# Performance work log

Measured on AMD Instinct MI355X. Metric: run time of the kernel, lower is better.

Reference implementation:

```python
import jax, jax.numpy as jnp
import numpy as np

B, S, H = 1, 1024, 2048
NH, NKV, HD = 32, 4, 128
E, K, I = 32, 8, 768
EPS = 1e-6
THETA = 10000.0


def setup_inputs() -> dict:
    key = jax.random.key(0)
    ks = jax.random.split(key, 12)
    s = 0.02
    return {
        "x": jax.random.normal(ks[0], (B, S, H), jnp.float32),
        "ln1_w": jnp.ones((H,), jnp.float32),
        "ln2_w": jnp.ones((H,), jnp.float32),
        "q_norm_w": jnp.ones((HD,), jnp.float32),
        "k_norm_w": jnp.ones((HD,), jnp.float32),
        "Wq": jax.random.normal(ks[1], (H, NH * HD), jnp.float32) * s,
        "Wk": jax.random.normal(ks[2], (H, NKV * HD), jnp.float32) * s,
        "Wv": jax.random.normal(ks[3], (H, NKV * HD), jnp.float32) * s,
        "Wo": jax.random.normal(ks[4], (NH * HD, H), jnp.float32) * s,
        "Wg": jax.random.normal(ks[5], (H, E), jnp.float32) * s,
        "W_gate_up": jax.random.normal(ks[6], (E, H, 2 * I), jnp.float32) * s,
        "W_down": jax.random.normal(ks[7], (E, I, H), jnp.float32) * s,
    }


def rms_norm(x, w, eps=EPS):
    var = jnp.mean(jnp.square(x), axis=-1, keepdims=True)
    return x * jax.lax.rsqrt(var + eps) * w


def rotate_half(x):
    x1, x2 = jnp.split(x, 2, axis=-1)
    return jnp.concatenate([-x2, x1], axis=-1)


def rope_cos_sin(seq_len, dtype):
    inv_freq = 1.0 / (THETA ** (jnp.arange(0, HD, 2, dtype=jnp.float32) / HD))
    freqs = jnp.arange(seq_len, dtype=jnp.float32)[:, None] * inv_freq[None, :]
    emb = jnp.concatenate([freqs, freqs], axis=-1)  # [S, HD]
    return jnp.cos(emb).astype(dtype)[None, :, None, :], jnp.sin(emb).astype(dtype)[None, :, None, :]


def attention(h, q_norm_w, k_norm_w, Wq, Wk, Wv, Wo):
    b, s, _ = h.shape
    q = (h @ Wq).reshape(b, s, NH, HD)
    k = (h @ Wk).reshape(b, s, NKV, HD)
    v = (h @ Wv).reshape(b, s, NKV, HD)
    # Qwen3 per-head q/k RMSNorm
    q = rms_norm(q, q_norm_w)
    k = rms_norm(k, k_norm_w)
    cos, sin = rope_cos_sin(s, h.dtype)
    q = q * cos + rotate_half(q) * sin
    k = k * cos + rotate_half(k) * sin
    # GQA: repeat kv heads
    rep = NH // NKV
    k = jnp.repeat(k, rep, axis=2)
    v = jnp.repeat(v, rep, axis=2)
    scale = HD ** -0.5
    scores = jnp.einsum('bqhd,bkhd->bhqk', q, k) * scale
    mask = jnp.tril(jnp.ones((s, s), bool))
    scores = jnp.where(mask[None, None], scores, jnp.array(-1e9, scores.dtype))
    attn = jax.nn.softmax(scores, axis=-1)
    out = jnp.einsum('bhqk,bkhd->bqhd', attn, v).reshape(b, s, NH * HD)
    return out @ Wo


def moe(h, Wg, W_gate_up, W_down):
    b, s, _ = h.shape
    t = h.reshape(b * s, H)
    logits = t @ Wg                          # [T, E]
    probs = jax.nn.softmax(logits, axis=-1)
    weights, indices = jax.lax.top_k(probs, K)  # [T, K] (no renormalization, per TopKRouter)
    combine = jnp.sum(jax.nn.one_hot(indices, E, dtype=t.dtype) * weights[..., None], axis=1)  # [T, E]
    gu = jnp.einsum('th,ehf->etf', t, W_gate_up)     # [E, T, 2I]
    gate, up = jnp.split(gu, 2, axis=-1)
    act = jax.nn.silu(gate) * up                     # [E, T, I]
    y = jnp.einsum('eti,eih->eth', act, W_down)      # [E, T, H]
    out = jnp.einsum('eth,te->th', y, combine)
    return out.reshape(b, s, H)


def reference(x, ln1_w, ln2_w, q_norm_w, k_norm_w, Wq, Wk, Wv, Wo, Wg, W_gate_up, W_down):
    h = x + attention(rms_norm(x, ln1_w), q_norm_w, k_norm_w, Wq, Wk, Wv, Wo)
    out = h + moe(rms_norm(h, ln2_w), Wg, W_gate_up, W_down)
    return out
```

## Files before the change

kernel.cpp:

```cpp
#include <hip/hip_runtime.h>
#include <hip/hip_bf16.h>


#define T_TOK 1024
#define HDIM  2048
#define NHEAD 32
#define NKVH  4
#define HD    128
#define NEXP  32
#define TOPK  8
#define IDIM  768

typedef __hip_bfloat16 bf16;

__device__ __forceinline__ float ld1(const float* p, size_t i) { return p[i]; }
__device__ __forceinline__ float ld1(const bf16* p, size_t i) { return __bfloat162float(p[i]); }

__global__ void detect_kernel(const unsigned* __restrict__ ln1w_bits, int* __restrict__ flag) {
  if (threadIdx.x == 0) flag[0] = (ln1w_bits[0] == 0x3F803F80u) ? 1 : 0;
}

template <typename Tx, typename Tw>
__device__ __forceinline__ void rms_body(const Tx* __restrict__ x, const Tw* __restrict__ w,
                                         float* __restrict__ out, float* red) {
  int t = blockIdx.x;
  const Tx* row = x + (size_t)t * HDIM;
  float ss = 0.f;
  for (int h = threadIdx.x; h < HDIM; h += 256) {
    float v = ld1(row, h);
    ss += v * v;
  }
#pragma unroll
  for (int off = 32; off; off >>= 1) ss += __shfl_down(ss, off);
  if ((threadIdx.x & 63) == 0) red[threadIdx.x >> 6] = ss;
  __syncthreads();
  float inv = rsqrtf((red[0] + red[1] + red[2] + red[3]) / (float)HDIM + 1e-6f);
  float* o = out + (size_t)t * HDIM;
  for (int h = threadIdx.x; h < HDIM; h += 256) o[h] = ld1(row, h) * inv * ld1(w, h);
}

__global__ void rmsnorm_dyn_kernel(const void* x, const void* w, float* out, const int* flag) {
  __shared__ float red[4];
  if (flag[0]) rms_body<bf16, bf16>((const bf16*)x, (const bf16*)w, out, red);
  else         rms_body<float, float>((const float*)x, (const float*)w, out, red);
}

__global__ void rmsnorm_f32_kernel(const float* x, const void* w, float* out, const int* flag) {
  __shared__ float red[4];
  if (flag[0]) rms_body<float, bf16>(x, (const bf16*)w, out, red);
  else         rms_body<float, float>(x, (const float*)w, out, red);
}

template <typename Tb>
__device__ __forceinline__ void gemm_body(const float* __restrict__ A, const Tb* __restrict__ B,
                                          float* __restrict__ C, const Tb* __restrict__ res,
                                          int N, int K, float* As , float* Bs) {
  int tid = threadIdx.x;
  int tx = tid & 15, ty = tid >> 4;
  int row0 = blockIdx.y * 64, col0 = blockIdx.x * 64;
  float acc[4][4] = {};
  for (int k0 = 0; k0 < K; k0 += 16) {
#pragma unroll
    for (int l = 0; l < 4; ++l) {
      int idx = tid + l * 256;
      int r = idx >> 4, c = idx & 15;
      As[c * 65 + r] = A[(size_t)(row0 + r) * K + k0 + c];
    }
#pragma unroll
    for (int l = 0; l < 4; ++l) {
      int idx = tid + l * 256;
      int r = idx >> 6, c = idx & 63;
      Bs[r * 65 + c] = ld1(B, (size_t)(k0 + r) * N + col0 + c);
    }
    __syncthreads();
#pragma unroll
    for (int k = 0; k < 16; ++k) {
      float av[4], bv[4];
#pragma unroll
      for (int i = 0; i < 4; ++i) av[i] = As[k * 65 + ty * 4 + i];
#pragma unroll
      for (int j = 0; j < 4; ++j) bv[j] = Bs[k * 65 + tx * 4 + j];
#pragma unroll
      for (int i = 0; i < 4; ++i)
#pragma unroll
        for (int j = 0; j < 4; ++j) acc[i][j] += av[i] * bv[j];
    }
    __syncthreads();
  }
#pragma unroll
  for (int i = 0; i < 4; ++i) {
    int r = row0 + ty * 4 + i;
#pragma unroll
    for (int j = 0; j < 4; ++j) {
      int c = col0 + tx * 4 + j;
      float v = acc[i][j];
      if (res) v += ld1(res, (size_t)r * N + c);
      C[(size_t)r * N + c] = v;
    }
  }
}

__global__ void gemm_kernel(const float* A, const void* B, float* C, const void* res,
                            int N, int K, const int* flag) {
  __shared__ float As[16 * 65];
  __shared__ float Bs[16 * 65];
  if (flag[0]) gemm_body<bf16>(A, (const bf16*)B, C, (const bf16*)res, N, K, As, Bs);
  else         gemm_body<float>(A, (const float*)B, C, (const float*)res, N, K, As, Bs);
}

template <typename Tw>
__device__ __forceinline__ void qkrope_body(float* __restrict__ q, float* __restrict__ k,
                                            const Tw* __restrict__ qw, const Tw* __restrict__ kw,
                                            float* sred, float* sh) {
  int t = blockIdx.x;
  int head = blockIdx.y;
  float* vec;
  const Tw* w;
  if (head < NHEAD) {
    vec = q + ((size_t)t * NHEAD + head) * HD;
    w = qw;
  } else {
    vec = k + ((size_t)t * NKVH + (head - NHEAD)) * HD;
    w = kw;
  }
  int d = threadIdx.x;
  float v = vec[d];
  float ss = v * v;
#pragma unroll
  for (int off = 32; off; off >>= 1) ss += __shfl_down(ss, off);
  if ((d & 63) == 0) sred[d >> 6] = ss;
  __syncthreads();
  float inv = rsqrtf((sred[0] + sred[1]) / (float)HD + 1e-6f);
  float nv = v * inv * ld1(w, d);
  sh[d] = nv;
  __syncthreads();
  float other = (d < 64) ? -sh[d + 64] : sh[d - 64];
  float inv_freq = powf(10000.f, -(float)(d & 63) / 64.f);
  float ang = (float)t * inv_freq;
  vec[d] = nv * cosf(ang) + other * sinf(ang);
}

__global__ void qk_norm_rope_kernel(float* q, float* k, const void* qw, const void* kw,
                                    const int* flag) {
  __shared__ float sred[2];
  __shared__ float sh[HD];
  if (flag[0]) qkrope_body<bf16>(q, k, (const bf16*)qw, (const bf16*)kw, sred, sh);
  else         qkrope_body<float>(q, k, (const float*)qw, (const float*)kw, sred, sh);
}

__global__ __launch_bounds__(256) void attn_tile_kernel(const float* q, const float* __restrict__ k,
                                                        const float* __restrict__ v, float* out) {
  __shared__ float Qs[64 * 132];
  __shared__ float KVs[64 * 132];
  int bid = blockIdx.x;
  int h = bid & 31;
  int p = bid >> 5;
  int kvh = h >> 3;
  int tid = threadIdx.x;
  int tx = tid & 15, ty = tid >> 4;
  int laneband = tid & 48;
  const float scale = 0.08838834764831845f;

  for (int half = 0; half < 2; ++half) {
    int qt = half ? (15 - p) : p;
    int q0 = qt * 64;
#pragma unroll
    for (int l = 0; l < 8; ++l) {
      int i = tid + l * 256;
      int r = i >> 5, c4 = (i & 31) * 4;
      float4 qv = *(const float4*)(q + (size_t)(q0 + r) * (NHEAD * HD) + h * HD + c4);
      qv.x *= scale; qv.y *= scale; qv.z *= scale; qv.w *= scale;
      *(float4*)&Qs[r * 132 + c4] = qv;
    }
    float m4[4] = {-1e30f, -1e30f, -1e30f, -1e30f};
    float l4[4] = {};
    float o[4][8] = {};
    __syncthreads();

    for (int kt = 0; kt <= qt; ++kt) {
      int j0 = kt * 64;
#pragma unroll
      for (int l = 0; l < 8; ++l) {
        int i = tid + l * 256;
        int r = i >> 5, c4 = (i & 31) * 4;
        *(float4*)&KVs[r * 132 + c4] =
            *(const float4*)(k + (size_t)(j0 + r) * (NKVH * HD) + kvh * HD + c4);
      }
      __syncthreads();
      float s[4][4] = {};
#pragma unroll 4
      for (int d4 = 0; d4 < 32; ++d4) {
        float4 av[4], bv[4];
#pragma unroll
        for (int i = 0; i < 4; ++i) av[i] = *(const float4*)&Qs[(ty + 16 * i) * 132 + d4 * 4];
#pragma unroll
        for (int j = 0; j < 4; ++j) bv[j] = *(const float4*)&KVs[(tx + 16 * j) * 132 + d4 * 4];
#pragma unroll
        for (int i = 0; i < 4; ++i)
#pragma unroll
          for (int j = 0; j < 4; ++j)
            s[i][j] += av[i].x * bv[j].x + av[i].y * bv[j].y + av[i].z * bv[j].z + av[i].w * bv[j].w;
      }
      if (kt == qt) {
#pragma unroll
        for (int i = 0; i < 4; ++i)
#pragma unroll
          for (int j = 0; j < 4; ++j)
            if (tx + 16 * j > ty + 16 * i) s[i][j] = -1e30f;
      }
      float rm[4], rs[4];
#pragma unroll
      for (int i = 0; i < 4; ++i)
        rm[i] = fmaxf(fmaxf(s[i][0], s[i][1]), fmaxf(s[i][2], s[i][3]));
#pragma unroll
      for (int mm = 1; mm < 16; mm <<= 1)
#pragma unroll
        for (int i = 0; i < 4; ++i) rm[i] = fmaxf(rm[i], __shfl_xor(rm[i], mm));
#pragma unroll
      for (int i = 0; i < 4; ++i) {
        float mn = fmaxf(m4[i], rm[i]);
        float corr = __expf(m4[i] - mn);
        m4[i] = mn;
        rs[i] = 0.f;
#pragma unroll
        for (int j = 0; j < 4; ++j) {
          s[i][j] = __expf(s[i][j] - mn);
          rs[i] += s[i][j];
        }
        l4[i] *= corr;
#pragma unroll
        for (int c = 0; c < 8; ++c) o[i][c] *= corr;
      }
#pragma unroll
      for (int mm = 1; mm < 16; mm <<= 1)
#pragma unroll
        for (int i = 0; i < 4; ++i) rs[i] += __shfl_xor(rs[i], mm);
#pragma unroll
      for (int i = 0; i < 4; ++i) l4[i] += rs[i];
      __syncthreads();
#pragma unroll
      for (int l = 0; l < 8; ++l) {
        int i = tid + l * 256;
        int r = i >> 5, c4 = (i & 31) * 4;
        *(float4*)&KVs[r * 132 + c4] =
            *(const float4*)(v + (size_t)(j0 + r) * (NKVH * HD) + kvh * HD + c4);
      }
      __syncthreads();
#pragma unroll
      for (int j = 0; j < 4; ++j) {
#pragma unroll 4
        for (int kks = 0; kks < 16; ++kks) {
          int kk = j * 16 + kks;
          int src = laneband | kks;
          float pb0 = __shfl(s[0][j], src);
          float pb1 = __shfl(s[1][j], src);
          float pb2 = __shfl(s[2][j], src);
          float pb3 = __shfl(s[3][j], src);
          float4 v0 = *(const float4*)&KVs[kk * 132 + tx * 8];
          float4 v1 = *(const float4*)&KVs[kk * 132 + tx * 8 + 4];
          o[0][0] += pb0 * v0.x; o[0][1] += pb0 * v0.y; o[0][2] += pb0 * v0.z; o[0][3] += pb0 * v0.w;
          o[0][4] += pb0 * v1.x; o[0][5] += pb0 * v1.y; o[0][6] += pb0 * v1.z; o[0][7] += pb0 * v1.w;
          o[1][0] += pb1 * v0.x; o[1][1] += pb1 * v0.y; o[1][2] += pb1 * v0.z; o[1][3] += pb1 * v0.w;
          o[1][4] += pb1 * v1.x; o[1][5] += pb1 * v1.y; o[1][6] += pb1 * v1.z; o[1][7] += pb1 * v1.w;
          o[2][0] += pb2 * v0.x; o[2][1] += pb2 * v0.y; o[2][2] += pb2 * v0.z; o[2][3] += pb2 * v0.w;
          o[2][4] += pb2 * v1.x; o[2][5] += pb2 * v1.y; o[2][6] += pb2 * v1.z; o[2][7] += pb2 * v1.w;
          o[3][0] += pb3 * v0.x; o[3][1] += pb3 * v0.y; o[3][2] += pb3 * v0.z; o[3][3] += pb3 * v0.w;
          o[3][4] += pb3 * v1.x; o[3][5] += pb3 * v1.y; o[3][6] += pb3 * v1.z; o[3][7] += pb3 * v1.w;
        }
      }
      __syncthreads();
    }
#pragma unroll
    for (int i = 0; i < 4; ++i) {
      float inv = 1.f / l4[i];
      int row = q0 + ty + 16 * i;
      float4 w0 = {o[i][0] * inv, o[i][1] * inv, o[i][2] * inv, o[i][3] * inv};
      float4 w1 = {o[i][4] * inv, o[i][5] * inv, o[i][6] * inv, o[i][7] * inv};
      *(float4*)(out + (size_t)row * (NHEAD * HD) + h * HD + tx * 8) = w0;
      *(float4*)(out + (size_t)row * (NHEAD * HD) + h * HD + tx * 8 + 4) = w1;
    }
    __syncthreads();
  }
}

template <typename Tw>
__device__ __forceinline__ void router_body(const float* __restrict__ h2,
                                            const Tw* __restrict__ Wg,
                                            float* __restrict__ combine,
                                            float* sh, float* probs) {
  int t = blockIdx.x;
  for (int h = threadIdx.x; h < HDIM; h += 64) sh[h] = h2[(size_t)t * HDIM + h];
  __syncthreads();
  int e = threadIdx.x;
  if (e < NEXP) {
    float acc = 0.f;
    for (int h = 0; h < HDIM; ++h) acc += sh[h] * ld1(Wg, (size_t)h * NEXP + e);
    probs[e] = acc;
  }
  __syncthreads();
  if (threadIdx.x == 0) {
    float mx = -1e30f;
    for (int i = 0; i < NEXP; ++i) mx = fmaxf(mx, probs[i]);
    float p[NEXP], sum = 0.f;
    for (int i = 0; i < NEXP; ++i) {
      p[i] = expf(probs[i] - mx);
      sum += p[i];
    }
    float o[NEXP];
    for (int i = 0; i < NEXP; ++i) {
      p[i] /= sum;
      o[i] = 0.f;
    }
    for (int kk = 0; kk < TOPK; ++kk) {
      int arg = 0;
      float best = p[0];
      for (int i = 1; i < NEXP; ++i)
        if (p[i] > best) { best = p[i]; arg = i; }
      o[arg] = best;
      p[arg] = -1.f;
    }
    for (int i = 0; i < NEXP; ++i) combine[(size_t)t * NEXP + i] = o[i];
  }
}

__global__ void router_kernel(const float* h2, const void* Wg, float* combine, const int* flag) {
  __shared__ float sh[HDIM];
  __shared__ float probs[NEXP];
  if (flag[0]) router_body<bf16>(h2, (const bf16*)Wg, combine, sh, probs);
  else         router_body<float>(h2, (const float*)Wg, combine, sh, probs);
}

__global__ void gather_kernel(const float* __restrict__ comb, int* __restrict__ cnt,
                              int* __restrict__ tok) {
  int e = blockIdx.x;
  __shared__ int lcnt;
  if (threadIdx.x == 0) lcnt = 0;
  __syncthreads();
  for (int t = threadIdx.x; t < T_TOK; t += 256) {
    if (comb[(size_t)t * NEXP + e] != 0.f) {
      int slot = atomicAdd(&lcnt, 1);
      tok[e * T_TOK + slot] = t;
    }
  }
  __syncthreads();
  if (threadIdx.x == 0) cnt[e] = lcnt;
}

__global__ void scan_kernel(const int* __restrict__ cnt, int* __restrict__ off) {
  if (threadIdx.x == 0) {
    int s = 0;
    for (int e = 0; e < NEXP; ++e) { off[e] = s; s += cnt[e]; }
  }
}

template <typename Tw>
__device__ __forceinline__ void gu_body(const float* __restrict__ h2, const Tw* __restrict__ Wgu,
                                        const int* __restrict__ cnt, const int* __restrict__ off,
                                        const int* __restrict__ tok, float* __restrict__ act,
                                        float* As, float* Bg, float* Bu, int* stok) {
  int e = blockIdx.z;
  int cn = cnt[e];
  int m0 = blockIdx.y * 64;
  if (m0 >= cn) return;
  int col0 = blockIdx.x * 64;
  int tid = threadIdx.x;
  if (tid < 64) stok[tid] = (m0 + tid < cn) ? tok[e * T_TOK + m0 + tid] : tok[e * T_TOK];
  __syncthreads();
  int tx = tid & 15, ty = tid >> 4;
  const Tw* wg = Wgu + (size_t)e * HDIM * (2 * IDIM);
  float ag[4][4] = {}, au[4][4] = {};
  for (int k0 = 0; k0 < HDIM; k0 += 16) {
#pragma unroll
    for (int l = 0; l < 4; ++l) {
      int idx = tid + l * 256;
      int r = idx >> 4, c = idx & 15;
      As[c * 65 + r] = h2[(size_t)stok[r] * HDIM + k0 + c];
    }
#pragma unroll
    for (int l = 0; l < 4; ++l) {
      int idx = tid + l * 256;
      int r = idx >> 6, c = idx & 63;
      const Tw* rowp = wg + (size_t)(k0 + r) * (2 * IDIM) + col0 + c;
      Bg[r * 65 + c] = ld1(rowp, 0);
      Bu[r * 65 + c] = ld1(rowp, IDIM);
    }
    __syncthreads();
#pragma unroll
    for (int k = 0; k < 16; ++k) {
      float av[4], bg[4], bu[4];
#pragma unroll
      for (int i = 0; i < 4; ++i) av[i] = As[k * 65 + ty * 4 + i];
#pragma unroll
      for (int j = 0; j < 4; ++j) { bg[j] = Bg[k * 65 + tx * 4 + j]; bu[j] = Bu[k * 65 + tx * 4 + j]; }
#pragma unroll
      for (int i = 0; i < 4; ++i)
#pragma unroll
        for (int j = 0; j < 4; ++j) { ag[i][j] += av[i] * bg[j]; au[i][j] += av[i] * bu[j]; }
    }
    __syncthreads();
  }
  int arow0 = off[e] + m0;
#pragma unroll
  for (int i = 0; i < 4; ++i) {
    int lr = ty * 4 + i;
    if (m0 + lr >= cn) continue;
    float* arow = act + (size_t)(arow0 + lr) * IDIM + col0;
#pragma unroll
    for (int j = 0; j < 4; ++j) {
      float g = ag[i][j], u = au[i][j];
      arow[tx * 4 + j] = (g / (1.f + expf(-g))) * u;
    }
  }
}

__global__ void moe_gu_kernel(const float* h2, const void* Wgu, const int* cnt, const int* off,
                              const int* tok, float* act, const int* flag) {
  __shared__ float As[16 * 65];
  __shared__ float Bg[16 * 65];
  __shared__ float Bu[16 * 65];
  __shared__ int stok[64];
  if (flag[0]) gu_body<bf16>(h2, (const bf16*)Wgu, cnt, off, tok, act, As, Bg, Bu, stok);
  else         gu_body<float>(h2, (const float*)Wgu, cnt, off, tok, act, As, Bg, Bu, stok);
}

template <typename Tw>
__device__ __forceinline__ void down_body(const float* __restrict__ act, const Tw* __restrict__ Wd,
                                          const float* __restrict__ comb,
                                          const int* __restrict__ cnt, const int* __restrict__ off,
                                          const int* __restrict__ tok, float* __restrict__ moeb,
                                          float* As, float* Bs, int* stok) {
  int e = blockIdx.z;
  int cn = cnt[e];
  int m0 = blockIdx.y * 64;
  if (m0 >= cn) return;
  int col0 = blockIdx.x * 64;
  int tid = threadIdx.x;
  if (tid < 64) stok[tid] = (m0 + tid < cn) ? tok[e * T_TOK + m0 + tid] : tok[e * T_TOK];
  __syncthreads();
  int tx = tid & 15, ty = tid >> 4;
  const Tw* wd = Wd + (size_t)e * IDIM * HDIM;
  const float* Ae = act + (size_t)(off[e] + m0) * IDIM;
  float acc[4][4] = {};
  for (int k0 = 0; k0 < IDIM; k0 += 16) {
#pragma unroll
    for (int l = 0; l < 4; ++l) {
      int idx = tid + l * 256;
      int r = idx >> 4, c = idx & 15;
      As[c * 65 + r] = (m0 + r < cn) ? Ae[(size_t)r * IDIM + k0 + c] : 0.f;
    }
#pragma unroll
    for (int l = 0; l < 4; ++l) {
      int idx = tid + l * 256;
      int r = idx >> 6, c = idx & 63;
      Bs[r * 65 + c] = ld1(wd, (size_t)(k0 + r) * HDIM + col0 + c);
    }
    __syncthreads();
#pragma unroll
    for (int k = 0; k < 16; ++k) {
      float av[4], bv[4];
#pragma unroll
      for (int i = 0; i < 4; ++i) av[i] = As[k * 65 + ty * 4 + i];
#pragma unroll
      for (int j = 0; j < 4; ++j) bv[j] = Bs[k * 65 + tx * 4 + j];
#pragma unroll
      for (int i = 0; i < 4; ++i)
#pragma unroll
        for (int j = 0; j < 4; ++j) acc[i][j] += av[i] * bv[j];
    }
    __syncthreads();
  }
#pragma unroll
  for (int i = 0; i < 4; ++i) {
    int lr = ty * 4 + i;
    if (m0 + lr >= cn) continue;
    int t = stok[lr];
    float wgt = comb[(size_t)t * NEXP + e];
#pragma unroll
    for (int j = 0; j < 4; ++j)
      atomicAdd(&moeb[(size_t)t * HDIM + col0 + tx * 4 + j], wgt * acc[i][j]);
  }
}

__global__ void moe_down_kernel(const float* act, const void* Wd, const float* comb,
                                const int* cnt, const int* off, const int* tok,
                                float* moeb, const int* flag) {
  __shared__ float As[16 * 65];
  __shared__ float Bs[16 * 65];
  __shared__ int stok[64];
  if (flag[0]) down_body<bf16>(act, (const bf16*)Wd, comb, cnt, off, tok, moeb, As, Bs, stok);
  else         down_body<float>(act, (const float*)Wd, comb, cnt, off, tok, moeb, As, Bs, stok);
}

template <typename Tw>
__device__ __forceinline__ void moe_body(const float* __restrict__ h2, const Tw* __restrict__ Wgu,
                                         const Tw* __restrict__ Wd, const float* __restrict__ combine,
                                         float* __restrict__ moe_out, float* sh, float* act) {
  int t = blockIdx.x;
  int e = blockIdx.y;
  float wgt = combine[(size_t)t * NEXP + e];
  if (wgt == 0.f) return;
  int tid = threadIdx.x;
  for (int h = tid; h < HDIM; h += 256) sh[h] = h2[(size_t)t * HDIM + h];
  __syncthreads();
  const Tw* wg = Wgu + (size_t)e * HDIM * (2 * IDIM);
#pragma unroll
  for (int c = 0; c < 3; ++c) {
    int i = c * 256 + tid;
    float g = 0.f, u = 0.f;
    for (int h = 0; h < HDIM; ++h) {
      const Tw* rowp = wg + (size_t)h * (2 * IDIM);
      float hv = sh[h];
      g += hv * ld1(rowp, i);
      u += hv * ld1(rowp, i + IDIM);
    }
    act[i] = (g / (1.f + expf(-g))) * u;
  }
  __syncthreads();
  const Tw* wd = Wd + (size_t)e * IDIM * HDIM;
#pragma unroll
  for (int c = 0; c < 8; ++c) {
    int h = c * 256 + tid;
    float acc = 0.f;
    for (int i = 0; i < IDIM; ++i) acc += act[i] * ld1(wd, (size_t)i * HDIM + h);
    atomicAdd(&moe_out[(size_t)t * HDIM + h], wgt * acc);
  }
}

__global__ void moe_kernel(const float* h2, const void* Wgu, const void* Wd,
                           const float* combine, float* moe_out, const int* flag) {
  __shared__ float sh[HDIM];
  __shared__ float act[IDIM];
  if (flag[0]) moe_body<bf16>(h2, (const bf16*)Wgu, (const bf16*)Wd, combine, moe_out, sh, act);
  else         moe_body<float>(h2, (const float*)Wgu, (const float*)Wd, combine, moe_out, sh, act);
}

__global__ void final_add_kernel(const float* __restrict__ hres, const float* __restrict__ moe,
                                 void* __restrict__ out, const int* flag) {
  size_t i = (size_t)blockIdx.x * 256 + threadIdx.x;
  float v = hres[i] + moe[i];
  if (flag[0]) ((bf16*)out)[i] = __float2bfloat16(v);
  else         ((float*)out)[i] = v;
}

extern "C" void kernel_launch(void* const* d_in, const int* in_sizes, int n_in,
                              void* d_out, int out_size, void* d_ws, size_t ws_size,
                              hipStream_t stream) {
  const void* x        = d_in[0];
  const void* ln1_w    = d_in[1];
  const void* ln2_w    = d_in[2];
  const void* q_norm_w = d_in[3];
  const void* k_norm_w = d_in[4];
  const void* Wq       = d_in[5];
  const void* Wk       = d_in[6];
  const void* Wv       = d_in[7];
  const void* Wo       = d_in[8];
  const void* Wg       = d_in[9];
  const void* Wgu      = d_in[10];
  const void* Wd       = d_in[11];

  int* flag   = (int*)d_ws;
  float* base = (float*)((char*)d_ws + 16);
  float* h1   = base;
  float* qbuf = h1 + (size_t)T_TOK * HDIM;
  float* kbuf = qbuf + (size_t)T_TOK * NHEAD * HD;
  float* vbuf = kbuf + (size_t)T_TOK * NKVH * HD;
  float* h2   = qbuf;
  float* comb = qbuf + (size_t)T_TOK * HDIM;
  float* moeb = comb + (size_t)T_TOK * NEXP;
  int*   cnt  = (int*)vbuf;
  int*   offp = cnt + 32;
  int*   tok  = cnt + 128;
  float* act  = vbuf + (size_t)T_TOK * NKVH * HD;

  size_t need = 16 + sizeof(float) * ((size_t)T_TOK * HDIM + (size_t)T_TOK * NHEAD * HD +
                                      2 * (size_t)T_TOK * NKVH * HD +
                                      (size_t)T_TOK * TOPK * IDIM);
  bool grouped = ws_size >= need;

  detect_kernel<<<1, 64, 0, stream>>>((const unsigned*)ln1_w, flag);
  rmsnorm_dyn_kernel<<<T_TOK, 256, 0, stream>>>(x, ln1_w, h1, flag);
  gemm_kernel<<<dim3(NHEAD * HD / 64, T_TOK / 64), 256, 0, stream>>>(h1, Wq, qbuf, nullptr, NHEAD * HD, HDIM, flag);
  gemm_kernel<<<dim3(NKVH * HD / 64, T_TOK / 64), 256, 0, stream>>>(h1, Wk, kbuf, nullptr, NKVH * HD, HDIM, flag);
  gemm_kernel<<<dim3(NKVH * HD / 64, T_TOK / 64), 256, 0, stream>>>(h1, Wv, vbuf, nullptr, NKVH * HD, HDIM, flag);
  qk_norm_rope_kernel<<<dim3(T_TOK, NHEAD + NKVH), HD, 0, stream>>>(qbuf, kbuf, q_norm_w, k_norm_w, flag);
  attn_tile_kernel<<<256, 256, 0, stream>>>(qbuf, kbuf, vbuf, qbuf);
  gemm_kernel<<<dim3(HDIM / 64, T_TOK / 64), 256, 0, stream>>>(qbuf, Wo, h1, x, HDIM, NHEAD * HD, flag);
  rmsnorm_f32_kernel<<<T_TOK, 256, 0, stream>>>(h1, ln2_w, h2, flag);
  hipMemsetAsync(moeb, 0, (size_t)T_TOK * HDIM * sizeof(float), stream);
  router_kernel<<<T_TOK, 64, 0, stream>>>(h2, Wg, comb, flag);
  if (grouped) {
    gather_kernel<<<NEXP, 256, 0, stream>>>(comb, cnt, tok);
    scan_kernel<<<1, 64, 0, stream>>>(cnt, offp);
    moe_gu_kernel<<<dim3(IDIM / 64, T_TOK / 64, NEXP), 256, 0, stream>>>(h2, Wgu, cnt, offp, tok, act, flag);
    moe_down_kernel<<<dim3(HDIM / 64, T_TOK / 64, NEXP), 256, 0, stream>>>(act, Wd, comb, cnt, offp, tok, moeb, flag);
  } else {
    moe_kernel<<<dim3(T_TOK, NEXP), 256, 0, stream>>>(h2, Wgu, Wd, comb, moeb, flag);
  }
  final_add_kernel<<<T_TOK * HDIM / 256, 256, 0, stream>>>(h1, moeb, d_out, flag);
}
```

Measured before the change: 3.991 ms.

## Use bf16 MFMA kernels for dense projections and grouped MoE GEMMs

Replaces the scalar-FMA shared-memory GEMMs for the Q/K/V/O projections and the grouped MoE gate-up and down GEMMs with MFMA 16x16x32 bf16 kernels. They stage fp32 activations as bf16 into swizzled LDS and read transposed B fragments with ds_read_b64_tr_b16. The goal is to move the dominant matmul work onto matrix cores with 128x64 tiles. The fp32 fallback paths are kept as separate kernels selected by the dtype flag, so each GEMM now launches twice, with one launch exiting early. Activations are rounded to bf16, which costs some precision.

After: 4.043 ms. About the same (+1.3%).

```diff
diff --git a/kernel.cpp b/kernel.cpp
--- a/kernel.cpp
+++ b/kernel.cpp
@@ -12,9 +12,23 @@
 #define IDIM  768
 
 typedef __hip_bfloat16 bf16;
+typedef short v8s __attribute__((ext_vector_type(8)));
+typedef float v4f __attribute__((ext_vector_type(4)));
+typedef int   v2i __attribute__((ext_vector_type(2)));
 
 __device__ __forceinline__ float ld1(const float* p, size_t i) { return p[i]; }
 __device__ __forceinline__ float ld1(const bf16* p, size_t i) { return __bfloat162float(p[i]); }
+
+__device__ __forceinline__ short f2b(float f) {
+  bf16 h = __float2bfloat16(f);
+  return *reinterpret_cast<short*>(&h);
+}
+
+__device__ __forceinline__ v8s punv8(v2i lo, v2i hi) {
+  union { struct { v2i a, b; } p; v8s s; } u;
+  u.p.a = lo; u.p.b = hi;
+  return u.s;
+}
 
 __global__ void detect_kernel(const unsigned* __restrict__ ln1w_bits, int* __restrict__ flag) {
   if (threadIdx.x == 0) flag[0] = (ln1w_bits[0] == 0x3F803F80u) ? 1 : 0;
@@ -51,10 +65,254 @@
   else         rms_body<float, float>(x, (const float*)w, out, red);
 }
 
-template <typename Tb>
-__device__ __forceinline__ void gemm_body(const float* __restrict__ A, const Tb* __restrict__ B,
-                                          float* __restrict__ C, const Tb* __restrict__ res,
-                                          int N, int K, float* As , float* Bs) {
+
+template <bool GATHER>
+__device__ __forceinline__ void stage_a(char* As, const float* __restrict__ A, int lda,
+                                        int k0, const int* __restrict__ rows, int nrows,
+                                        int tid) {
+#pragma unroll
+  for (int l = 0; l < 4; ++l) {
+    int g = tid + l * 256;
+    int row = g >> 3;
+    int k8 = (g & 7) * 8;
+    int sr = (row < nrows) ? row : 0;
+    const float* src;
+    if constexpr (GATHER) src = A + (size_t)rows[sr] * lda + k0 + k8;
+    else                  src = A + (size_t)sr * lda + k0 + k8;
+    float4 f0 = *(const float4*)src;
+    float4 f1 = *(const float4*)(src + 4);
+    v8s val;
+    val[0] = f2b(f0.x); val[1] = f2b(f0.y); val[2] = f2b(f0.z); val[3] = f2b(f0.w);
+    val[4] = f2b(f1.x); val[5] = f2b(f1.y); val[6] = f2b(f1.z); val[7] = f2b(f1.w);
+    unsigned byte = ((unsigned)(row * 128 + k8 * 2)) ^ ((unsigned)((row & 7) << 4));
+    *(v8s*)(As + byte) = val;
+  }
+}
+
+__device__ __forceinline__ void stage_b(char* Bs, const bf16* __restrict__ W, int ldb,
+                                        int k0, int n0, int tid) {
+#pragma unroll
+  for (int p = 0; p < 2; ++p) {
+    int idx = tid + p * 256;
+    int k = idx >> 3;
+    int n8 = (idx & 7) * 8;
+    v8s val = *(const v8s*)(W + (size_t)(k0 + k) * ldb + n0 + n8);
+    unsigned byte = (unsigned)((((n8 >> 4) * 16 + (k >> 2)) * 128) + (k & 3) * 32 + (n8 & 15) * 2);
+    *(v8s*)(Bs + byte) = val;
+  }
+}
+
+template <bool DUAL>
+__device__ __forceinline__ void mfma_bk(const char* As, const char* B0, const char* B1,
+                                        int lane, int wr, int wc,
+                                        v4f acc0[4][2], v4f acc1[4][2]) {
+  unsigned aswz = (unsigned)((lane & 7) << 4);
+  unsigned abase = (unsigned)((wr * 64 + (lane & 15)) * 128 + ((lane >> 4) * 16));
+#pragma unroll
+  for (int kc = 0; kc < 2; ++kc) {
+    v8s a[4];
+#pragma unroll
+    for (int mf = 0; mf < 4; ++mf)
+      a[mf] = *(const v8s*)(As + ((abase + mf * 2048 + kc * 64) ^ aswz));
+    unsigned bofs = (unsigned)((((wc * 2) * 16 + kc * 8) + (lane >> 4)) * 128);
+    unsigned a00 = (unsigned)(size_t)B0 + bofs;
+    unsigned a01 = a00 + 2048;
+    v2i l00, h00, l01, h01;
+    if constexpr (DUAL) {
+      unsigned a10 = (unsigned)(size_t)B1 + bofs;
+      unsigned a11 = a10 + 2048;
+      v2i l10, h10, l11, h11;
+      asm volatile(
+          "ds_read_b64_tr_b16 %0, %8\n\t"
+          "ds_read_b64_tr_b16 %1, %8 offset:128\n\t"
+          "ds_read_b64_tr_b16 %2, %9\n\t"
+          "ds_read_b64_tr_b16 %3, %9 offset:128\n\t"
+          "ds_read_b64_tr_b16 %4, %10\n\t"
+          "ds_read_b64_tr_b16 %5, %10 offset:128\n\t"
+          "ds_read_b64_tr_b16 %6, %11\n\t"
+          "ds_read_b64_tr_b16 %7, %11 offset:128\n\t"
+          "s_waitcnt lgkmcnt(0)"
+          : "=&v"(l00), "=&v"(h00), "=&v"(l01), "=&v"(h01),
+            "=&v"(l10), "=&v"(h10), "=&v"(l11), "=&v"(h11)
+          : "v"(a00), "v"(a01), "v"(a10), "v"(a11));
+      __builtin_amdgcn_sched_barrier(0);
+      v8s b00 = punv8(l00, h00), b01 = punv8(l01, h01);
+      v8s b10 = punv8(l10, h10), b11 = punv8(l11, h11);
+#pragma unroll
+      for (int mf = 0; mf < 4; ++mf) {
+        acc0[mf][0] = __builtin_amdgcn_mfma_f32_16x16x32_bf16(a[mf], b00, acc0[mf][0], 0, 0, 0);
+        acc0[mf][1] = __builtin_amdgcn_mfma_f32_16x16x32_bf16(a[mf], b01, acc0[mf][1], 0, 0, 0);
+        acc1[mf][0] = __builtin_amdgcn_mfma_f32_16x16x32_bf16(a[mf], b10, acc1[mf][0], 0, 0, 0);
+        acc1[mf][1] = __builtin_amdgcn_mfma_f32_16x16x32_bf16(a[mf], b11, acc1[mf][1], 0, 0, 0);
+      }
+    } else {
+      asm volatile(
+          "ds_read_b64_tr_b16 %0, %4\n\t"
+          "ds_read_b64_tr_b16 %1, %4 offset:128\n\t"
+          "ds_read_b64_tr_b16 %2, %5\n\t"
+          "ds_read_b64_tr_b16 %3, %5 offset:128\n\t"
+          "s_waitcnt lgkmcnt(0)"
+          : "=&v"(l00), "=&v"(h00), "=&v"(l01), "=&v"(h01)
+          : "v"(a00), "v"(a01));
+      __builtin_amdgcn_sched_barrier(0);
+      v8s b00 = punv8(l00, h00), b01 = punv8(l01, h01);
+#pragma unroll
+      for (int mf = 0; mf < 4; ++mf) {
+        acc0[mf][0] = __builtin_amdgcn_mfma_f32_16x16x32_bf16(a[mf], b00, acc0[mf][0], 0, 0, 0);
+        acc0[mf][1] = __builtin_amdgcn_mfma_f32_16x16x32_bf16(a[mf], b01, acc0[mf][1], 0, 0, 0);
+      }
+    }
+  }
+}
+
+__global__ __launch_bounds__(256) void mfma_dense_kernel(const float* __restrict__ A,
+                                                         const void* __restrict__ Bv,
+                                                         float* __restrict__ C,
+                                                         const void* __restrict__ resv,
+                                                         int N, int K,
+                                                         const int* __restrict__ flag) {
+  if (!flag[0]) return;
+  __shared__ __align__(128) char smem[24 * 1024];
+  char* As = smem;
+  char* Bs = smem + 16 * 1024;
+  const bf16* B = (const bf16*)Bv;
+  const bf16* res = (const bf16*)resv;
+  int tid = threadIdx.x;
+  int row0 = blockIdx.y * 128, col0 = blockIdx.x * 64;
+  int lane = tid & 63, wid = tid >> 6, wr = wid >> 1, wc = wid & 1;
+  v4f acc[4][2] = {};
+  const float* Ab = A + (size_t)row0 * K;
+  for (int k0 = 0; k0 < K; k0 += 64) {
+    stage_a<false>(As, Ab, K, k0, nullptr, 128, tid);
+    stage_b(Bs, B, N, k0, col0, tid);
+    __syncthreads();
+    mfma_bk<false>(As, Bs, nullptr, lane, wr, wc, acc, acc);
+    __syncthreads();
+  }
+#pragma unroll
+  for (int mf = 0; mf < 4; ++mf)
+#pragma unroll
+    for (int r = 0; r < 4; ++r) {
+      int lr = wr * 64 + mf * 16 + (lane >> 4) * 4 + r;
+#pragma unroll
+      for (int nf = 0; nf < 2; ++nf) {
+        int col = col0 + wc * 32 + nf * 16 + (lane & 15);
+        float v = acc[mf][nf][r];
+        if (res) v += ld1(res, (size_t)(row0 + lr) * N + col);
+        C[(size_t)(row0 + lr) * N + col] = v;
+      }
+    }
+}
+
+__global__ __launch_bounds__(256) void mfma_gu_kernel(const float* __restrict__ h2,
+                                                      const void* __restrict__ Wguv,
+                                                      const int* __restrict__ cnt,
+                                                      const int* __restrict__ off,
+                                                      const int* __restrict__ tok,
+                                                      float* __restrict__ act,
+                                                      const int* __restrict__ flag) {
+  if (!flag[0]) return;
+  int e = blockIdx.z;
+  int cn = cnt[e];
+  int m0 = blockIdx.y * 128;
+  if (m0 >= cn) return;
+  __shared__ __align__(128) char smem[32 * 1024];
+  __shared__ int stok[128];
+  char* As = smem;
+  char* Bg = smem + 16 * 1024;
+  char* Bu = smem + 24 * 1024;
+  int tid = threadIdx.x;
+  if (tid < 128) stok[tid] = (m0 + tid < cn) ? tok[e * T_TOK + m0 + tid] : tok[e * T_TOK];
+  int col0 = blockIdx.x * 64;
+  const bf16* wg = (const bf16*)Wguv + (size_t)e * HDIM * (2 * IDIM);
+  int lane = tid & 63, wid = tid >> 6, wr = wid >> 1, wc = wid & 1;
+  v4f accG[4][2] = {}, accU[4][2] = {};
+  __syncthreads();
+  for (int k0 = 0; k0 < HDIM; k0 += 64) {
+    stage_a<true>(As, h2, HDIM, k0, stok, 128, tid);
+    stage_b(Bg, wg, 2 * IDIM, k0, col0, tid);
+    stage_b(Bu, wg, 2 * IDIM, k0, col0 + IDIM, tid);
+    __syncthreads();
+    mfma_bk<true>(As, Bg, Bu, lane, wr, wc, accG, accU);
+    __syncthreads();
+  }
+  int arow0 = off[e] + m0;
+#pragma unroll
+  for (int mf = 0; mf < 4; ++mf)
+#pragma unroll
+    for (int r = 0; r < 4; ++r) {
+      int lr = wr * 64 + mf * 16 + (lane >> 4) * 4 + r;
+      if (m0 + lr < cn) {
+#pragma unroll
+        for (int nf = 0; nf < 2; ++nf) {
+          float g = accG[mf][nf][r], u = accU[mf][nf][r];
+          int col = col0 + wc * 32 + nf * 16 + (lane & 15);
+          act[(size_t)(arow0 + lr) * IDIM + col] = (g / (1.f + expf(-g))) * u;
+        }
+      }
+    }
+}
+
+__global__ __launch_bounds__(256) void mfma_down_kernel(const float* __restrict__ act,
+                                                        const void* __restrict__ Wdv,
+                                                        const float* __restrict__ comb,
+                                                        const int* __restrict__ cnt,
+                                                        const int* __restrict__ off,
+                                                        const int* __restrict__ tok,
+                                                        float* __restrict__ moeb,
+                                                        const int* __restrict__ flag) {
+  if (!flag[0]) return;
+  int e = blockIdx.z;
+  int cn = cnt[e];
+  int m0 = blockIdx.y * 128;
+  if (m0 >= cn) return;
+  __shared__ __align__(128) char smem[24 * 1024];
+  __shared__ int stok[128];
+  __shared__ float swgt[128];
+  char* As = smem;
+  char* Bs = smem + 16 * 1024;
+  int tid = threadIdx.x;
+  if (tid < 128) {
+    int t = (m0 + tid < cn) ? tok[e * T_TOK + m0 + tid] : tok[e * T_TOK];
+    stok[tid] = t;
+    swgt[tid] = comb[(size_t)t * NEXP + e];
+  }
+  int col0 = blockIdx.x * 64;
+  const bf16* wd = (const bf16*)Wdv + (size_t)e * IDIM * HDIM;
+  const float* Ab = act + (size_t)(off[e] + m0) * IDIM;
+  int nrows = min(128, cn - m0);
+  int lane = tid & 63, wid = tid >> 6, wr = wid >> 1, wc = wid & 1;
+  v4f acc[4][2] = {};
+  __syncthreads();
+  for (int k0 = 0; k0 < IDIM; k0 += 64) {
+    stage_a<false>(As, Ab, IDIM, k0, nullptr, nrows, tid);
+    stage_b(Bs, wd, HDIM, k0, col0, tid);
+    __syncthreads();
+    mfma_bk<false>(As, Bs, nullptr, lane, wr, wc, acc, acc);
+    __syncthreads();
+  }
+#pragma unroll
+  for (int mf = 0; mf < 4; ++mf)
+#pragma unroll
+    for (int r = 0; r < 4; ++r) {
+      int lr = wr * 64 + mf * 16 + (lane >> 4) * 4 + r;
+      if (lr < nrows) {
+        int t = stok[lr];
+        float wgt = swgt[lr];
+#pragma unroll
+        for (int nf = 0; nf < 2; ++nf) {
+          int col = col0 + wc * 32 + nf * 16 + (lane & 15);
+          atomicAdd(&moeb[(size_t)t * HDIM + col], wgt * acc[mf][nf][r]);
+        }
+      }
+    }
+}
+
+__global__ void gemm_f32_kernel(const float* A, const float* B, float* C, const float* res,
+                                int N, int K, const int* flag) {
+  if (flag[0]) return;
+  __shared__ float As[16 * 65];
+  __shared__ float Bs[16 * 65];
   int tid = threadIdx.x;
   int tx = tid & 15, ty = tid >> 4;
   int row0 = blockIdx.y * 64, col0 = blockIdx.x * 64;
@@ -70,7 +328,7 @@
     for (int l = 0; l < 4; ++l) {
       int idx = tid + l * 256;
       int r = idx >> 6, c = idx & 63;
-      Bs[r * 65 + c] = ld1(B, (size_t)(k0 + r) * N + col0 + c);
+      Bs[r * 65 + c] = B[(size_t)(k0 + r) * N + col0 + c];
     }
     __syncthreads();
 #pragma unroll
@@ -94,18 +352,134 @@
     for (int j = 0; j < 4; ++j) {
       int c = col0 + tx * 4 + j;
       float v = acc[i][j];
-      if (res) v += ld1(res, (size_t)r * N + c);
+      if (res) v += res[(size_t)r * N + c];
       C[(size_t)r * N + c] = v;
     }
   }
 }
 
-__global__ void gemm_kernel(const float* A, const void* B, float* C, const void* res,
-                            int N, int K, const int* flag) {
+__global__ void gu_f32_kernel(const float* __restrict__ h2, const float* __restrict__ Wgu,
+                              const int* __restrict__ cnt, const int* __restrict__ off,
+                              const int* __restrict__ tok, float* __restrict__ act,
+                              const int* flag) {
+  if (flag[0]) return;
+  __shared__ float As[16 * 65];
+  __shared__ float Bg[16 * 65];
+  __shared__ float Bu[16 * 65];
+  __shared__ int stok[64];
+  int e = blockIdx.z;
+  int cn = cnt[e];
+  int m0 = blockIdx.y * 64;
+  if (m0 >= cn) return;
+  int col0 = blockIdx.x * 64;
+  int tid = threadIdx.x;
+  if (tid < 64) stok[tid] = (m0 + tid < cn) ? tok[e * T_TOK + m0 + tid] : tok[e * T_TOK];
+  __syncthreads();
+  int tx = tid & 15, ty = tid >> 4;
+  const float* wg = Wgu + (size_t)e * HDIM * (2 * IDIM);
+  float ag[4][4] = {}, au[4][4] = {};
+  for (int k0 = 0; k0 < HDIM; k0 += 16) {
+#pragma unroll
+    for (int l = 0; l < 4; ++l) {
+      int idx = tid + l * 256;
+      int r = idx >> 4, c = idx & 15;
+      As[c * 65 + r] = h2[(size_t)stok[r] * HDIM + k0 + c];
+    }
+#pragma unroll
+    for (int l = 0; l < 4; ++l) {
+      int idx = tid + l * 256;
+      int r = idx >> 6, c = idx & 63;
+      const float* rowp = wg + (size_t)(k0 + r) * (2 * IDIM) + col0 + c;
+      Bg[r * 65 + c] = rowp[0];
+      Bu[r * 65 + c] = rowp[IDIM];
+    }
+    __syncthreads();
+#pragma unroll
+    for (int k = 0; k < 16; ++k) {
+      float av[4], bg[4], bu[4];
+#pragma unroll
+      for (int i = 0; i < 4; ++i) av[i] = As[k * 65 + ty * 4 + i];
+#pragma unroll
+      for (int j = 0; j < 4; ++j) { bg[j] = Bg[k * 65 + tx * 4 + j]; bu[j] = Bu[k * 65 + tx * 4 + j]; }
+#pragma unroll
+      for (int i = 0; i < 4; ++i)
+#pragma unroll
+        for (int j = 0; j < 4; ++j) { ag[i][j] += av[i] * bg[j]; au[i][j] += av[i] * bu[j]; }
+    }
+    __syncthreads();
+  }
+  int arow0 = off[e] + m0;
+#pragma unroll
+  for (int i = 0; i < 4; ++i) {
+    int lr = ty * 4 + i;
+    if (m0 + lr >= cn) continue;
+    float* arow = act + (size_t)(arow0 + lr) * IDIM + col0;
+#pragma unroll
+    for (int j = 0; j < 4; ++j) {
+      float g = ag[i][j], u = au[i][j];
+      arow[tx * 4 + j] = (g / (1.f + expf(-g))) * u;
+    }
+  }
+}
+
+__global__ void down_f32_kernel(const float* __restrict__ act, const float* __restrict__ Wd,
+                                const float* __restrict__ comb, const int* __restrict__ cnt,
+                                const int* __restrict__ off, const int* __restrict__ tok,
+                                float* __restrict__ moeb, const int* flag) {
+  if (flag[0]) return;
   __shared__ float As[16 * 65];
   __shared__ float Bs[16 * 65];
-  if (flag[0]) gemm_body<bf16>(A, (const bf16*)B, C, (const bf16*)res, N, K, As, Bs);
-  else         gemm_body<float>(A, (const float*)B, C, (const float*)res, N, K, As, Bs);
+  __shared__ int stok[64];
+  int e = blockIdx.z;
+  int cn = cnt[e];
+  int m0 = blockIdx.y * 64;
+  if (m0 >= cn) return;
+  int col0 = blockIdx.x * 64;
+  int tid = threadIdx.x;
+  if (tid < 64) stok[tid] = (m0 + tid < cn) ? tok[e * T_TOK + m0 + tid] : tok[e * T_TOK];
+  __syncthreads();
+  int tx = tid & 15, ty = tid >> 4;
+  const float* wd = Wd + (size_t)e * IDIM * HDIM;
+  const float* Ae = act + (size_t)(off[e] + m0) * IDIM;
+  float acc[4][4] = {};
+  for (int k0 = 0; k0 < IDIM; k0 += 16) {
+#pragma unroll
+    for (int l = 0; l < 4; ++l) {
+      int idx = tid + l * 256;
+      int r = idx >> 4, c = idx & 15;
+      As[c * 65 + r] = (m0 + r < cn) ? Ae[(size_t)r * IDIM + k0 + c] : 0.f;
+    }
+#pragma unroll
+    for (int l = 0; l < 4; ++l) {
+      int idx = tid + l * 256;
+      int r = idx >> 6, c = idx & 63;
+      Bs[r * 65 + c] = wd[(size_t)(k0 + r) * HDIM + col0 + c];
+    }
+    __syncthreads();
+#pragma unroll
+    for (int k = 0; k < 16; ++k) {
+      float av[4], bv[4];
+#pragma unroll
+      for (int i = 0; i < 4; ++i) av[i] = As[k * 65 + ty * 4 + i];
+#pragma unroll
+      for (int j = 0; j < 4; ++j) bv[j] = Bs[k * 65 + tx * 4 + j];
+#pragma unroll
+      for (int i = 0; i < 4; ++i)
+#pragma unroll
+        for (int j = 0; j < 4; ++j) acc[i][j] += av[i] * bv[j];
+    }
+    __syncthreads();
+  }
+#pragma unroll
+  for (int i = 0; i < 4; ++i) {
+    int lr = ty * 4 + i;
+    if (m0 + lr >= cn) continue;
+    int t = stok[lr];
+    float wgt = comb[(size_t)t * NEXP + e];
+#pragma unroll
+    for (int j = 0; j < 4; ++j)
+      atomicAdd(&moeb[(size_t)t * HDIM + col0 + tx * 4 + j], wgt * acc[i][j]);
+  }
 }
 
 template <typename Tw>
@@ -354,144 +728,6 @@
 }
 
 template <typename Tw>
-__device__ __forceinline__ void gu_body(const float* __restrict__ h2, const Tw* __restrict__ Wgu,
-                                        const int* __restrict__ cnt, const int* __restrict__ off,
-                                        const int* __restrict__ tok, float* __restrict__ act,
-                                        float* As, float* Bg, float* Bu, int* stok) {
-  int e = blockIdx.z;
-  int cn = cnt[e];
-  int m0 = blockIdx.y * 64;
-  if (m0 >= cn) return;
-  int col0 = blockIdx.x * 64;
-  int tid = threadIdx.x;
-  if (tid < 64) stok[tid] = (m0 + tid < cn) ? tok[e * T_TOK + m0 + tid] : tok[e * T_TOK];
-  __syncthreads();
-  int tx = tid & 15, ty = tid >> 4;
-  const Tw* wg = Wgu + (size_t)e * HDIM * (2 * IDIM);
-  float ag[4][4] = {}, au[4][4] = {};
-  for (int k0 = 0; k0 < HDIM; k0 += 16) {
-#pragma unroll
-    for (int l = 0; l < 4; ++l) {
-      int idx = tid + l * 256;
-      int r = idx >> 4, c = idx & 15;
-      As[c * 65 + r] = h2[(size_t)stok[r] * HDIM + k0 + c];
-    }
-#pragma unroll
-    for (int l = 0; l < 4; ++l) {
-      int idx = tid + l * 256;
-      int r = idx >> 6, c = idx & 63;
-      const Tw* rowp = wg + (size_t)(k0 + r) * (2 * IDIM) + col0 + c;
-      Bg[r * 65 + c] = ld1(rowp, 0);
-      Bu[r * 65 + c] = ld1(rowp, IDIM);
-    }
-    __syncthreads();
-#pragma unroll
-    for (int k = 0; k < 16; ++k) {
-      float av[4], bg[4], bu[4];
-#pragma unroll
-      for (int i = 0; i < 4; ++i) av[i] = As[k * 65 + ty * 4 + i];
-#pragma unroll
-      for (int j = 0; j < 4; ++j) { bg[j] = Bg[k * 65 + tx * 4 + j]; bu[j] = Bu[k * 65 + tx * 4 + j]; }
-#pragma unroll
-      for (int i = 0; i < 4; ++i)
-#pragma unroll
-        for (int j = 0; j < 4; ++j) { ag[i][j] += av[i] * bg[j]; au[i][j] += av[i] * bu[j]; }
-    }
-    __syncthreads();
-  }
-  int arow0 = off[e] + m0;
-#pragma unroll
-  for (int i = 0; i < 4; ++i) {
-    int lr = ty * 4 + i;
-    if (m0 + lr >= cn) continue;
-    float* arow = act + (size_t)(arow0 + lr) * IDIM + col0;
-#pragma unroll
-    for (int j = 0; j < 4; ++j) {
-      float g = ag[i][j], u = au[i][j];
-      arow[tx * 4 + j] = (g / (1.f + expf(-g))) * u;
-    }
-  }
-}
-
-__global__ void moe_gu_kernel(const float* h2, const void* Wgu, const int* cnt, const int* off,
-                              const int* tok, float* act, const int* flag) {
-  __shared__ float As[16 * 65];
-  __shared__ float Bg[16 * 65];
-  __shared__ float Bu[16 * 65];
-  __shared__ int stok[64];
-  if (flag[0]) gu_body<bf16>(h2, (const bf16*)Wgu, cnt, off, tok, act, As, Bg, Bu, stok);
-  else         gu_body<float>(h2, (const float*)Wgu, cnt, off, tok, act, As, Bg, Bu, stok);
-}
-
-template <typename Tw>
-__device__ __forceinline__ void down_body(const float* __restrict__ act, const Tw* __restrict__ Wd,
-                                          const float* __restrict__ comb,
-                                          const int* __restrict__ cnt, const int* __restrict__ off,
-                                          const int* __restrict__ tok, float* __restrict__ moeb,
-                                          float* As, float* Bs, int* stok) {
-  int e = blockIdx.z;
-  int cn = cnt[e];
-  int m0 = blockIdx.y * 64;
-  if (m0 >= cn) return;
-  int col0 = blockIdx.x * 64;
-  int tid = threadIdx.x;
-  if (tid < 64) stok[tid] = (m0 + tid < cn) ? tok[e * T_TOK + m0 + tid] : tok[e * T_TOK];
-  __syncthreads();
-  int tx = tid & 15, ty = tid >> 4;
-  const Tw* wd = Wd + (size_t)e * IDIM * HDIM;
-  const float* Ae = act + (size_t)(off[e] + m0) * IDIM;
-  float acc[4][4] = {};
-  for (int k0 = 0; k0 < IDIM; k0 += 16) {
-#pragma unroll
-    for (int l = 0; l < 4; ++l) {
-      int idx = tid + l * 256;
-      int r = idx >> 4, c = idx & 15;
-      As[c * 65 + r] = (m0 + r < cn) ? Ae[(size_t)r * IDIM + k0 + c] : 0.f;
-    }
-#pragma unroll
-    for (int l = 0; l < 4; ++l) {
-      int idx = tid + l * 256;
-      int r = idx >> 6, c = idx & 63;
-      Bs[r * 65 + c] = ld1(wd, (size_t)(k0 + r) * HDIM + col0 + c);
-    }
-    __syncthreads();
-#pragma unroll
-    for (int k = 0; k < 16; ++k) {
-      float av[4], bv[4];
-#pragma unroll
-      for (int i = 0; i < 4; ++i) av[i] = As[k * 65 + ty * 4 + i];
-#pragma unroll
-      for (int j = 0; j < 4; ++j) bv[j] = Bs[k * 65 + tx * 4 + j];
-#pragma unroll
-      for (int i = 0; i < 4; ++i)
-#pragma unroll
-        for (int j = 0; j < 4; ++j) acc[i][j] += av[i] * bv[j];
-    }
-    __syncthreads();
-  }
-#pragma unroll
-  for (int i = 0; i < 4; ++i) {
-    int lr = ty * 4 + i;
-    if (m0 + lr >= cn) continue;
-    int t = stok[lr];
-    float wgt = comb[(size_t)t * NEXP + e];
-#pragma unroll
-    for (int j = 0; j < 4; ++j)
-      atomicAdd(&moeb[(size_t)t * HDIM + col0 + tx * 4 + j], wgt * acc[i][j]);
-  }
-}
-
-__global__ void moe_down_kernel(const float* act, const void* Wd, const float* comb,
-                                const int* cnt, const int* off, const int* tok,
-                                float* moeb, const int* flag) {
-  __shared__ float As[16 * 65];
-  __shared__ float Bs[16 * 65];
-  __shared__ int stok[64];
-  if (flag[0]) down_body<bf16>(act, (const bf16*)Wd, comb, cnt, off, tok, moeb, As, Bs, stok);
-  else         down_body<float>(act, (const float*)Wd, comb, cnt, off, tok, moeb, As, Bs, stok);
-}
-
-template <typename Tw>
 __device__ __forceinline__ void moe_body(const float* __restrict__ h2, const Tw* __restrict__ Wgu,
                                          const Tw* __restrict__ Wd, const float* __restrict__ combine,
                                          float* __restrict__ moe_out, float* sh, float* act) {
@@ -579,20 +815,26 @@
 
   detect_kernel<<<1, 64, 0, stream>>>((const unsigned*)ln1_w, flag);
   rmsnorm_dyn_kernel<<<T_TOK, 256, 0, stream>>>(x, ln1_w, h1, flag);
-  gemm_kernel<<<dim3(NHEAD * HD / 64, T_TOK / 64), 256, 0, stream>>>(h1, Wq, qbuf, nullptr, NHEAD * HD, HDIM, flag);
-  gemm_kernel<<<dim3(NKVH * HD / 64, T_TOK / 64), 256, 0, stream>>>(h1, Wk, kbuf, nullptr, NKVH * HD, HDIM, flag);
-  gemm_kernel<<<dim3(NKVH * HD / 64, T_TOK / 64), 256, 0, stream>>>(h1, Wv, vbuf, nullptr, NKVH * HD, HDIM, flag);
+  mfma_dense_kernel<<<dim3(NHEAD * HD / 64, T_TOK / 128), 256, 0, stream>>>(h1, Wq, qbuf, nullptr, NHEAD * HD, HDIM, flag);
+  mfma_dense_kernel<<<dim3(NKVH * HD / 64, T_TOK / 128), 256, 0, stream>>>(h1, Wk, kbuf, nullptr, NKVH * HD, HDIM, flag);
+  mfma_dense_kernel<<<dim3(NKVH * HD / 64, T_TOK / 128), 256, 0, stream>>>(h1, Wv, vbuf, nullptr, NKVH * HD, HDIM, flag);
+  gemm_f32_kernel<<<dim3(NHEAD * HD / 64, T_TOK / 64), 256, 0, stream>>>(h1, (const float*)Wq, qbuf, nullptr, NHEAD * HD, HDIM, flag);
+  gemm_f32_kernel<<<dim3(NKVH * HD / 64, T_TOK / 64), 256, 0, stream>>>(h1, (const float*)Wk, kbuf, nullptr, NKVH * HD, HDIM, flag);
+  gemm_f32_kernel<<<dim3(NKVH * HD / 64, T_TOK / 64), 256, 0, stream>>>(h1, (const float*)Wv, vbuf, nullptr, NKVH * HD, HDIM, flag);
   qk_norm_rope_kernel<<<dim3(T_TOK, NHEAD + NKVH), HD, 0, stream>>>(qbuf, kbuf, q_norm_w, k_norm_w, flag);
   attn_tile_kernel<<<256, 256, 0, stream>>>(qbuf, kbuf, vbuf, qbuf);
-  gemm_kernel<<<dim3(HDIM / 64, T_TOK / 64), 256, 0, stream>>>(qbuf, Wo, h1, x, HDIM, NHEAD * HD, flag);
+  mfma_dense_kernel<<<dim3(HDIM / 64, T_TOK / 128), 256, 0, stream>>>(qbuf, Wo, h1, x, HDIM, NHEAD * HD, flag);
+  gemm_f32_kernel<<<dim3(HDIM / 64, T_TOK / 64), 256, 0, stream>>>(qbuf, (const float*)Wo, h1, (const float*)x, HDIM, NHEAD * HD, flag);
   rmsnorm_f32_kernel<<<T_TOK, 256, 0, stream>>>(h1, ln2_w, h2, flag);
   hipMemsetAsync(moeb, 0, (size_t)T_TOK * HDIM * sizeof(float), stream);
   router_kernel<<<T_TOK, 64, 0, stream>>>(h2, Wg, comb, flag);
   if (grouped) {
     gather_kernel<<<NEXP, 256, 0, stream>>>(comb, cnt, tok);
     scan_kernel<<<1, 64, 0, stream>>>(cnt, offp);
-    moe_gu_kernel<<<dim3(IDIM / 64, T_TOK / 64, NEXP), 256, 0, stream>>>(h2, Wgu, cnt, offp, tok, act, flag);
-    moe_down_kernel<<<dim3(HDIM / 64, T_TOK / 64, NEXP), 256, 0, stream>>>(act, Wd, comb, cnt, offp, tok, moeb, flag);
+    mfma_gu_kernel<<<dim3(IDIM / 64, T_TOK / 128, NEXP), 256, 0, stream>>>(h2, Wgu, cnt, offp, tok, act, flag);
+    gu_f32_kernel<<<dim3(IDIM / 64, T_TOK / 64, NEXP), 256, 0, stream>>>(h2, (const float*)Wgu, cnt, offp, tok, act, flag);
+    mfma_down_kernel<<<dim3(HDIM / 64, T_TOK / 128, NEXP), 256, 0, stream>>>(act, Wd, comb, cnt, offp, tok, moeb, flag);
+    down_f32_kernel<<<dim3(HDIM / 64, T_TOK / 64, NEXP), 256, 0, stream>>>(act, (const float*)Wd, comb, cnt, offp, tok, moeb, flag);
   } else {
     moe_kernel<<<dim3(T_TOK, NEXP), 256, 0, stream>>>(h2, Wgu, Wd, comb, moeb, flag);
   }
```
